# Performance work log

Measured on AMD Instinct MI355X. Metric: run time of the kernel, lower is better.

The kernel has to match this reference:

```python
import math
import jax, jax.numpy as jnp
import numpy as np

B, C, H, W = 8, 256, 32, 32
NH, DK, DV = 8, 32, 32
EPS = 1e-6


def mish(x):
    return x * jnp.tanh(jax.nn.softplus(x))


def grouped_conv1x1(x, w, b, groups):
    # x: (B, Cin, N); w: (Cout, Cin//groups); b: (Cout,)
    Bb, Cin, N = x.shape
    Cout = w.shape[0]
    xg = x.reshape(Bb, groups, Cin // groups, N)
    wg = w.reshape(groups, Cout // groups, Cin // groups)
    y = jnp.einsum('bgin,goi->bgon', xg, wg).reshape(Bb, Cout, N)
    return y + b[None, :, None]


def conv_block(x, w, b, s, beta, groups):
    # 1x1 conv -> BatchNorm (eval: running mean 0 / var 1 => affine) -> Mish
    y = grouped_conv1x1(x, w, b, groups)
    y = s[None, :, None] * y + beta[None, :, None]
    return mish(y)


def setup_inputs() -> dict:
    key = jax.random.key(0)
    ks = jax.random.split(key, 8)
    inp = {
        'x': jax.random.normal(ks[0], (B, C, H, W), dtype=jnp.float32),
        'q_w': jax.random.normal(ks[1], (NH * DK, C // NH), dtype=jnp.float32) * 0.05,
        'q_b': jnp.zeros((NH * DK,), jnp.float32),
        'q_s': jnp.ones((NH * DK,), jnp.float32),
        'q_beta': jnp.zeros((NH * DK,), jnp.float32),
        'k_w': jax.random.normal(ks[2], (NH * DK, C // NH), dtype=jnp.float32) * 0.05,
        'k_b': jnp.zeros((NH * DK,), jnp.float32),
        'k_s': jnp.ones((NH * DK,), jnp.float32),
        'k_beta': jnp.zeros((NH * DK,), jnp.float32),
        'v_w': jax.random.normal(ks[3], (NH * DV, C // NH), dtype=jnp.float32) * 0.05,
        'v_b': jnp.zeros((NH * DV,), jnp.float32),
        'v_s': jnp.ones((NH * DV,), jnp.float32),
        'v_beta': jnp.zeros((NH * DV,), jnp.float32),
        'f_w': jax.random.normal(ks[4], (C, NH * DV), dtype=jnp.float32) * 0.05,
        'f_b': jnp.zeros((C,), jnp.float32),
        'f_s': jnp.ones((C,), jnp.float32),
        'f_beta': jnp.zeros((C,), jnp.float32),
    }
    return inp


def _forward(x, q_w, q_b, q_s, q_beta, k_w, k_b, k_s, k_beta,
             v_w, v_b, v_s, v_beta, f_w, f_b, f_s, f_beta):
    b, c, h, w = x.shape
    n = h * w
    temp = math.sqrt(c / NH)
    xf = x.reshape(b, c, n)

    q = conv_block(xf, q_w, q_b, q_s, q_beta, NH).reshape(b, NH, DK, n) / temp
    k = conv_block(xf, k_w, k_b, k_s, k_beta, NH).reshape(b, NH, DK, n)
    v = conv_block(xf, v_w, v_b, v_s, v_beta, NH).reshape(b, NH, DV, n)

    # cosine-distance attention (all heads vectorized); identical math to the
    # torch broadcast/repeat version but computed via normalized dot products.
    qn = jnp.sqrt(jnp.sum(q * q, axis=2))  # (b, nh, n)
    kn = jnp.sqrt(jnp.sum(k * k, axis=2))
    dot = jnp.einsum('bhdn,bhdm->bhnm', q, k)  # (b, nh, n, n)
    denom = jnp.maximum(qn[:, :, :, None] * kn[:, :, None, :], EPS)
    cos = jnp.clip(dot / denom, -1.0 + 1e-6, 1.0 - 1e-6)
    attn = jax.nn.softmax(1.0 - jnp.arccos(cos) / math.pi, axis=-1)

    # out[..., d, i] = sum_m v[..., d, m] * attn[..., i, m]
    out = jnp.einsum('bhdm,bhnm->bhdn', v, attn).reshape(b, NH * DV, n)

    y = conv_block(out, f_w, f_b, f_s, f_beta, 1).reshape(b, c, h, w) + x

    # extract_attn_map (no_grad in original)
    am = jnp.sum(jnp.mean(attn, axis=1), axis=1)  # (b, n)
    mn = jnp.min(am, axis=1, keepdims=True)
    mx = jnp.max(am, axis=1, keepdims=True)
    am = ((am - mn) / (mx - mn)).reshape(b, h, w)
    return y, jax.lax.stop_gradient(am)


def reference(x, q_w, q_b, q_s, q_beta, k_w, k_b, k_s, k_beta,
              v_w, v_b, v_s, v_beta, f_w, f_b, f_s, f_beta):
    return _forward(x, q_w, q_b, q_s, q_beta, k_w, k_b, k_s, k_beta,
                    v_w, v_b, v_s, v_beta, f_w, f_b, f_s, f_beta)
```

## Files before the change

### kernel.cpp

```cpp
#include <hip/hip_runtime.h>
#include <math.h>

#define B_   8
#define C_   256
#define NH_  8
#define N_   1024
#define LOG2E    1.4426950408889634f

typedef __attribute__((ext_vector_type(8))) short bf16x8;
typedef __attribute__((ext_vector_type(4))) float f32x4;
typedef __attribute__((ext_vector_type(2))) float f32x2;
typedef unsigned short u16;
typedef unsigned int u32;

#define AS1 __attribute__((address_space(1)))
#define AS3 __attribute__((address_space(3)))

__device__ __forceinline__ f32x4 mfma16(bf16x8 a, bf16x8 b, f32x4 c) {
    return __builtin_amdgcn_mfma_f32_16x16x32_bf16(a, b, c, 0, 0, 0);
}
__device__ __forceinline__ u32 bf16r(float x) {
    u32 b = __float_as_uint(x);
    return (b + 0x7fffu + ((b >> 16) & 1u)) >> 16;
}
__device__ __forceinline__ float mish_fast(float x) {
    float e  = __builtin_amdgcn_exp2f(fminf(x, 30.f) * LOG2E);
    float nm = e * (e + 2.f);
    return x * nm * __builtin_amdgcn_rcpf(nm + 2.f);
}
__device__ __forceinline__ f32x2 splat2(float v) { return (f32x2){v, v}; }
__device__ __forceinline__ f32x2 fexp_poly2(f32x2 c) {
    c = __builtin_elementwise_min(
            __builtin_elementwise_max(c, splat2(-0.999999f)), splat2(0.999999f));
    f32x2 u = c * c;
    f32x2 p = __builtin_elementwise_fma(splat2(1.7809920f), u, splat2(-3.7571968f));
    f32x2 q = __builtin_elementwise_fma(splat2(6.3713280f), u, splat2(-15.1427584f));
    p = __builtin_elementwise_fma(p, u, splat2(2.8140000f));
    q = __builtin_elementwise_fma(q, u, splat2(13.1518784f));
    p = __builtin_elementwise_fma(p, u, splat2(-0.8122592f));
    q = __builtin_elementwise_fma(q, u, splat2(-4.8903712f));
    p = __builtin_elementwise_fma(p, u, splat2(0.1705120f));
    q = __builtin_elementwise_fma(q, u, splat2(0.8441120f));
    p = __builtin_elementwise_fma(p, u, splat2(1.6473155f));
    q = __builtin_elementwise_fma(q, u, splat2(0.4936541f));
    return __builtin_elementwise_fma(c, q, p);
}

__global__ __launch_bounds__(256) void qkvpack_kernel(
    const float* __restrict__ x,
    const float* __restrict__ qw, const float* __restrict__ qb2,
    const float* __restrict__ qs, const float* __restrict__ qbeta,
    const float* __restrict__ kw, const float* __restrict__ kb2,
    const float* __restrict__ ks, const float* __restrict__ kbeta,
    const float* __restrict__ vw, const float* __restrict__ vb2,
    const float* __restrict__ vs, const float* __restrict__ vbeta,
    uint4* __restrict__ qpk, uint4* __restrict__ kpk, u16* __restrict__ vbf,
    const float* __restrict__ fw, u16* __restrict__ wbf)
{
    int blk = blockIdx.x;
    if (blk >= 768) {
        int id = (blk - 768) * 1024 + threadIdx.x;
#pragma unroll
        for (int j = 0; j < 4; ++j) { int p = id + j * 256; wbf[p] = (u16)bf16r(fw[p]); }
        return;
    }
    int type = blk >> 8;
    int sub = blk & 255;
    int nt = sub & 3, g = (sub >> 2) & 7, b = sub >> 5;
    int n = nt * 256 + threadIdx.x;
    int bh = b * 8 + g;
    const float* xp = x + ((size_t)b * C_ + g * 32) * N_ + n;
    float xv[32];
#pragma unroll
    for (int i = 0; i < 32; ++i) xv[i] = xp[(size_t)i * N_];

    const float *w, *bb, *sc, *bt;
    if (type == 0)      { w = qw; bb = qb2; sc = qs; bt = qbeta; }
    else if (type == 1) { w = kw; bb = kb2; sc = ks; bt = kbeta; }
    else                { w = vw; bb = vb2; sc = vs; bt = vbeta; }

    float y[32];
#pragma unroll
    for (int co = 0; co < 32; ++co) {
        int cg = g * 32 + co;
        float acc = 0.f;
#pragma unroll
        for (int i = 0; i < 32; ++i)
            acc = fmaf(xv[i], w[cg * 32 + i], acc);
        y[co] = mish_fast(sc[cg] * (acc + bb[cg]) + bt[cg]);
    }

    if (type == 2) {
#pragma unroll
        for (int co = 0; co < 32; ++co)
            vbf[((size_t)bh * 32 + co) * N_ + n] = (u16)bf16r(y[co]);
        return;
    }
    float s2 = 0.f;
#pragma unroll
    for (int d = 0; d < 32; ++d) s2 = fmaf(y[d], y[d], s2);
    float inv = __builtin_amdgcn_rsqf(fmaxf(s2, 1e-24f));
    u32 wp[16];
#pragma unroll
    for (int d = 0; d < 16; ++d)
        wp[d] = bf16r(y[2 * d] * inv) | (bf16r(y[2 * d + 1] * inv) << 16);
    uint4* dst = (type == 0 ? qpk : kpk) + ((size_t)bh * N_ + n) * 4;
#pragma unroll
    for (int j = 0; j < 4; ++j)
        dst[j] = make_uint4(wp[4 * j], wp[4 * j + 1], wp[4 * j + 2], wp[4 * j + 3]);
}

__global__ __launch_bounds__(256) void attn_kernel(
    const u16* __restrict__ qpk, const u16* __restrict__ kpk,
    const u16* __restrict__ vbf,
    u16* __restrict__ aout_bt, float* __restrict__ ampart)
{
    __shared__ __align__(16) u16 Kc[512 * 8];
    __shared__ __align__(16) u16 Vc[512 * 8];
    __shared__ __align__(16) u16 Ps[4][16 * 136];
    __shared__ __align__(16) float amW[N_];

    const int tid  = threadIdx.x;
    const int wave = tid >> 6, lane = tid & 63;
    const int l15 = lane & 15, lg = lane >> 4;
    const int swz = (blockIdx.x & 7) * 128 + (blockIdx.x >> 3);
    const int itile = swz & 15, bh = swz >> 4;
    const int h = bh & 7, bidx = bh >> 3;
    const int i0 = itile * 64;

    const char* ksrc = (const char*)(kpk + (size_t)bh * N_ * 32);
    const char* vsrc = (const char*)(vbf + (size_t)bh * 32 * N_);
    const char* qsrc = (const char*)(qpk + (size_t)bh * N_ * 32);

    for (int j = tid; j < N_; j += 256) amW[j] = 0.f;

    const int kj0 = tid >> 7, km0g = tid & 127;
    const int kj1 = (256 + tid) >> 7, km1g = (256 + tid) & 127;
    const int vd0 = tid >> 4, vg0 = tid & 15;
    const int vd1 = (256 + tid) >> 4, vg1 = (256 + tid) & 15;
    const size_t koff0 = (size_t)km0g * 64 + kj0 * 16;
    const size_t koff1 = (size_t)km1g * 64 + kj1 * 16;
    const size_t voff0 = (size_t)vd0 * 2048 + ((vg0 ^ (vd0 & 7)) << 4);
    const size_t voff1 = (size_t)vd1 * 2048 + ((vg1 ^ (vd1 & 7)) << 4);

    bf16x8 aq = *(const bf16x8*)(qsrc + (size_t)(i0 + wave * 16 + l15) * 64 + lg * 16);

    const char* kfb = (const char*)Kc + lg * 2048 + l15 * 16;

    uint4 kreg0 = *(const uint4*)(ksrc + koff0);
    uint4 kreg1 = *(const uint4*)(ksrc + koff1);
    f32x2 rsL = {0.f, 0.f}, rsH = {0.f, 0.f};
    for (int ch = 0; ch < 8; ++ch) {
        *(uint4*)((char*)Kc + tid * 16)         = kreg0;
        *(uint4*)((char*)Kc + (256 + tid) * 16) = kreg1;
        if (ch < 7) {
            kreg0 = *(const uint4*)(ksrc + (size_t)(ch + 1) * 8192 + koff0);
            kreg1 = *(const uint4*)(ksrc + (size_t)(ch + 1) * 8192 + koff1);
        }
        asm volatile("s_waitcnt lgkmcnt(0)" ::: "memory");
        __builtin_amdgcn_sched_barrier(0);
        __builtin_amdgcn_s_barrier();
        __builtin_amdgcn_sched_barrier(0);
#pragma unroll
        for (int t = 0; t < 8; ++t) {
            bf16x8 bk = *(const bf16x8*)(kfb + t * 256);
            f32x4 cf = {0.f, 0.f, 0.f, 0.f};
            cf = mfma16(aq, bk, cf);
            rsL += fexp_poly2((f32x2){cf[0], cf[1]});
            rsH += fexp_poly2((f32x2){cf[2], cf[3]});
        }
        asm volatile("s_waitcnt lgkmcnt(0)" ::: "memory");
        __builtin_amdgcn_sched_barrier(0);
        __builtin_amdgcn_s_barrier();
        __builtin_amdgcn_sched_barrier(0);
    }
    float rinv[4];
    {
        float rr[4] = {rsL.x, rsL.y, rsH.x, rsH.y};
#pragma unroll
        for (int r = 0; r < 4; ++r) {
            float s = rr[r];
            s += __shfl_xor(s, 1); s += __shfl_xor(s, 2);
            s += __shfl_xor(s, 4); s += __shfl_xor(s, 8);
            rinv[r] = __builtin_amdgcn_rcpf(s);
        }
    }
    f32x2 rinvL = {rinv[0], rinv[1]}, rinvH = {rinv[2], rinv[3]};

    f32x4 o0 = {0.f, 0.f, 0.f, 0.f}, o1 = {0.f, 0.f, 0.f, 0.f};
    char*       psw = (char*)&Ps[wave][0] + lg * 1088 + l15 * 2;
    const char* pab = (const char*)&Ps[wave][0] + l15 * 272 + lg * 16;
    const char* vfb = (const char*)Vc + l15 * 256;
    const int   vkey = l15 & 7;

    kreg0 = *(const uint4*)(ksrc + koff0);
    kreg1 = *(const uint4*)(ksrc + koff1);
    uint4 vreg0 = *(const uint4*)(vsrc + voff0);
    uint4 vreg1 = *(const uint4*)(vsrc + voff1);

    for (int ch = 0; ch < 8; ++ch) {
        int m0 = ch * 128;
        *(uint4*)((char*)Kc + tid * 16)         = kreg0;
        *(uint4*)((char*)Kc + (256 + tid) * 16) = kreg1;
        *(uint4*)((char*)Vc + tid * 16)         = vreg0;
        *(uint4*)((char*)Vc + (256 + tid) * 16) = vreg1;
        if (ch < 7) {
            kreg0 = *(const uint4*)(ksrc + (size_t)(ch + 1) * 8192 + koff0);
            kreg1 = *(const uint4*)(ksrc + (size_t)(ch + 1) * 8192 + koff1);
            vreg0 = *(const uint4*)(vsrc + (size_t)(ch + 1) * 256 + voff0);
            vreg1 = *(const uint4*)(vsrc + (size_t)(ch + 1) * 256 + voff1);
        }
        asm volatile("s_waitcnt lgkmcnt(0)" ::: "memory");
        __builtin_amdgcn_sched_barrier(0);
        __builtin_amdgcn_s_barrier();
        __builtin_amdgcn_sched_barrier(0);

#pragma unroll
        for (int t = 0; t < 8; ++t) {
            bf16x8 bk = *(const bf16x8*)(kfb + t * 256);
            f32x4 cf = {0.f, 0.f, 0.f, 0.f};
            cf = mfma16(aq, bk, cf);
            f32x2 fL = fexp_poly2((f32x2){cf[0], cf[1]});
            f32x2 fH = fexp_poly2((f32x2){cf[2], cf[3]});
            *(u16*)(psw + 0 * 272 + t * 32) = (u16)bf16r(fL.x);
            *(u16*)(psw + 1 * 272 + t * 32) = (u16)bf16r(fL.y);
            *(u16*)(psw + 2 * 272 + t * 32) = (u16)bf16r(fH.x);
            *(u16*)(psw + 3 * 272 + t * 32) = (u16)bf16r(fH.y);
            f32x2 cs2 = fL * rinvL;
            cs2 = __builtin_elementwise_fma(fH, rinvH, cs2);
            float csum = cs2.x + cs2.y;
            csum += __shfl_xor(csum, 16);
            csum += __shfl_xor(csum, 32);
            if (lane < 16) atomicAdd(&amW[m0 + t * 16 + l15], csum);
        }
        asm volatile("s_waitcnt lgkmcnt(0)" ::: "memory");
        __builtin_amdgcn_sched_barrier(0);
#pragma unroll
        for (int kss = 0; kss < 4; ++kss) {
            bf16x8 pa = *(const bf16x8*)(pab + kss * 64);
            const char* va = vfb + (((kss * 4 + lg) ^ vkey) << 4);
            bf16x8 v0 = *(const bf16x8*)va;
            bf16x8 v1 = *(const bf16x8*)(va + 4096);
            o0 = mfma16(pa, v0, o0);
            o1 = mfma16(pa, v1, o1);
        }
        asm volatile("s_waitcnt lgkmcnt(0)" ::: "memory");
        __builtin_amdgcn_sched_barrier(0);
        __builtin_amdgcn_s_barrier();
        __builtin_amdgcn_sched_barrier(0);
    }
    __syncthreads();

    {
        u16* oT = (u16*)Ps;
#pragma unroll
        for (int r = 0; r < 4; ++r) {
            int irow = wave * 16 + lg * 4 + r;
            oT[irow * 40 + l15]      = (u16)bf16r(o0[r] * rinv[r]);
            oT[irow * 40 + 16 + l15] = (u16)bf16r(o1[r] * rinv[r]);
        }
    }
    __syncthreads();
    {
        const u16* oT = (const u16*)Ps;
        int row = tid >> 2, c4 = tid & 3;
        uint4 val = *(const uint4*)((const char*)oT + row * 80 + c4 * 16);
        int n = i0 + row;
        int g = h * 4 + c4;
        size_t dst = ((size_t)(bidx * N_ + n) << 9) + ((size_t)((g ^ (row & 7)) << 4));
        *(uint4*)((char*)aout_bt + dst) = val;
    }
#pragma unroll
    for (int j2 = 0; j2 < 4; ++j2)
        ampart[(size_t)swz * N_ + tid + 256 * j2] = amW[tid + 256 * j2];
}

__global__ __launch_bounds__(256) void fconv_kernel(
    const u16* __restrict__ aout_bt, const u16* __restrict__ wbf,
    const float* __restrict__ x,
    const float* __restrict__ fs, const float* __restrict__ fb,
    const float* __restrict__ fbeta, float* __restrict__ y,
    const float* __restrict__ ampart, float* __restrict__ outAm)
{
    __shared__ __align__(16) u16 As[32 * 256];
    __shared__ float rmn[256], rmx[256];
    const int tid = threadIdx.x;

    if (blockIdx.x >= 256) {
        int b = blockIdx.x - 256;
        const float* base = ampart + (size_t)b * 128 * N_;
        float s[4] = {0.f, 0.f, 0.f, 0.f};
        for (int p = 0; p < 128; ++p) {
#pragma unroll
            for (int c2 = 0; c2 < 4; ++c2)
                s[c2] += base[(size_t)p * N_ + tid + 256 * c2];
        }
        float mn = fminf(fminf(s[0], s[1]), fminf(s[2], s[3]));
        float mx = fmaxf(fmaxf(s[0], s[1]), fmaxf(s[2], s[3]));
        rmn[tid] = mn; rmx[tid] = mx;
        __syncthreads();
        for (int off = 128; off >= 1; off >>= 1) {
            if (tid < off) {
                rmn[tid] = fminf(rmn[tid], rmn[tid + off]);
                rmx[tid] = fmaxf(rmx[tid], rmx[tid + off]);
            }
            __syncthreads();
        }
        mn = rmn[0]; mx = rmx[0];
        float inv = 1.f / (mx - mn);
#pragma unroll
        for (int c2 = 0; c2 < 4; ++c2)
            outAm[(size_t)b * N_ + tid + 256 * c2] = (s[c2] - mn) * inv;
        return;
    }

    const int wave = tid >> 6, lane = tid & 63;
    const int l15 = lane & 15, lg = lane >> 4;
    const int b  = blockIdx.x >> 5;
    const int n0 = (blockIdx.x & 31) * 32;

    const char* asrc = (const char*)aout_bt + ((size_t)(b * N_ + n0) << 9);
#pragma unroll
    for (int p = 0; p < 4; ++p) {
        int g = p * 256 + wave * 64 + lane;
        __builtin_amdgcn_global_load_lds(
            (const AS1 void*)(asrc + g * 16),
            (AS3 void*)((char*)As + ((p * 256 + wave * 64) << 4)), 16, 0, 0);
    }
    __syncthreads();

    f32x4 acc[4][2];
#pragma unroll
    for (int f = 0; f < 4; ++f)
#pragma unroll
        for (int fn = 0; fn < 2; ++fn) acc[f][fn] = (f32x4){0.f, 0.f, 0.f, 0.f};

    const int cobase = wave * 64;
#pragma unroll
    for (int kk = 0; kk < 8; ++kk) {
        bf16x8 af[2];
#pragma unroll
        for (int fn = 0; fn < 2; ++fn) {
            int nf = fn * 16 + l15;
            af[fn] = *(const bf16x8*)((const char*)As + nf * 512 +
                                      (((kk * 4 + lg) ^ (nf & 7)) << 4));
        }
#pragma unroll
        for (int f = 0; f < 4; ++f) {
            bf16x8 wf = *(const bf16x8*)(wbf + (size_t)(cobase + f * 16 + l15) * 256 + kk * 32 + lg * 8);
            acc[f][0] = mfma16(wf, af[0], acc[f][0]);
            acc[f][1] = mfma16(wf, af[1], acc[f][1]);
        }
    }

#pragma unroll
    for (int f = 0; f < 4; ++f) {
#pragma unroll
        for (int r = 0; r < 4; ++r) {
            int co = cobase + f * 16 + lg * 4 + r;
            float sc = fs[co], bb = fb[co], bt = fbeta[co];
#pragma unroll
            for (int fn = 0; fn < 2; ++fn) {
                int n = n0 + fn * 16 + l15;
                size_t oid = ((size_t)(b * C_ + co) << 10) + n;
                y[oid] = mish_fast(sc * (acc[f][fn][r] + bb) + bt) + x[oid];
            }
        }
    }
}

extern "C" void kernel_launch(void* const* d_in, const int* in_sizes, int n_in,
                              void* d_out, int out_size, void* d_ws, size_t ws_size,
                              hipStream_t stream)
{
    const float* x     = (const float*)d_in[0];
    const float* q_w   = (const float*)d_in[1];
    const float* q_b   = (const float*)d_in[2];
    const float* q_s   = (const float*)d_in[3];
    const float* q_be  = (const float*)d_in[4];
    const float* k_w   = (const float*)d_in[5];
    const float* k_b   = (const float*)d_in[6];
    const float* k_s   = (const float*)d_in[7];
    const float* k_be  = (const float*)d_in[8];
    const float* v_w   = (const float*)d_in[9];
    const float* v_b   = (const float*)d_in[10];
    const float* v_s   = (const float*)d_in[11];
    const float* v_be  = (const float*)d_in[12];
    const float* f_w   = (const float*)d_in[13];
    const float* f_b   = (const float*)d_in[14];
    const float* f_s   = (const float*)d_in[15];
    const float* f_be  = (const float*)d_in[16];

    float* y_out  = (float*)d_out;
    float* am_out = (float*)d_out + (size_t)B_ * C_ * N_;

    char* w = (char*)d_ws;
    u16*   qpk     = (u16*)w;    w += (size_t)B_ * NH_ * N_ * 64;
    u16*   kpk     = (u16*)w;    w += (size_t)B_ * NH_ * N_ * 64;
    u16*   vbf     = (u16*)w;    w += (size_t)B_ * C_ * N_ * 2;
    u16*   aout_bt = (u16*)w;    w += (size_t)B_ * N_ * C_ * 2;
    float* ampart  = (float*)w;  w += (size_t)B_ * NH_ * 16 * N_ * 4;
    u16*   wbf     = (u16*)w;

    qkvpack_kernel<<<832, 256, 0, stream>>>(
        x, q_w, q_b, q_s, q_be, k_w, k_b, k_s, k_be,
        v_w, v_b, v_s, v_be, (uint4*)qpk, (uint4*)kpk, vbf, f_w, wbf);

    attn_kernel<<<B_ * NH_ * 16, 256, 0, stream>>>(
        qpk, kpk, vbf, aout_bt, ampart);

    fconv_kernel<<<264, 256, 0, stream>>>(
        aout_bt, wbf, x, f_s, f_b, f_be, y_out, ampart, am_out);
}
```

Measured before the change: 104.5 us.

## Double-buffer K/V tiles in LDS with direct global_load_lds transfers

Replaces the register-staged global-to-LDS copies of K and V chunks with `__builtin_amdgcn_global_load_lds` DMA into double-buffered LDS tiles. The next chunk is prefetched into the alternate buffer while the current one is consumed. This cuts the two barriers per chunk down to one vmcnt wait plus barrier. The aim is to save VGPRs and VALU store instructions and to overlap memory latency with the MFMA and exp work. In exchange it doubles the K/V LDS footprint, which may lower occupancy, and the new scheme depends on careful vmcnt/barrier ordering being correct.

```diff
diff --git a/kernel.cpp b/kernel.cpp
--- a/kernel.cpp
+++ b/kernel.cpp
@@ -115,8 +115,8 @@
     const u16* __restrict__ vbf,
     u16* __restrict__ aout_bt, float* __restrict__ ampart)
 {
-    __shared__ __align__(16) u16 Kc[512 * 8];
-    __shared__ __align__(16) u16 Vc[512 * 8];
+    __shared__ __align__(16) u16 Kb[2][512 * 8];
+    __shared__ __align__(16) u16 Vb[2][512 * 8];
     __shared__ __align__(16) u16 Ps[4][16 * 136];
     __shared__ __align__(16) float amW[N_];
 
@@ -134,33 +134,44 @@
 
     for (int j = tid; j < N_; j += 256) amW[j] = 0.f;
 
-    const int kj0 = tid >> 7, km0g = tid & 127;
-    const int kj1 = (256 + tid) >> 7, km1g = (256 + tid) & 127;
-    const int vd0 = tid >> 4, vg0 = tid & 15;
-    const int vd1 = (256 + tid) >> 4, vg1 = (256 + tid) & 15;
-    const size_t koff0 = (size_t)km0g * 64 + kj0 * 16;
-    const size_t koff1 = (size_t)km1g * 64 + kj1 * 16;
+    const int g0 = wave * 64 + lane, g1 = 256 + wave * 64 + lane;
+    const size_t koff0 = (size_t)(g0 & 127) * 64 + (size_t)(g0 >> 7) * 16;
+    const size_t koff1 = (size_t)(g1 & 127) * 64 + (size_t)(g1 >> 7) * 16;
+    const int vd0 = g0 >> 4, vg0 = g0 & 15, vd1 = g1 >> 4, vg1 = g1 & 15;
     const size_t voff0 = (size_t)vd0 * 2048 + ((vg0 ^ (vd0 & 7)) << 4);
     const size_t voff1 = (size_t)vd1 * 2048 + ((vg1 ^ (vd1 & 7)) << 4);
+    const int dst0 = (wave * 64) << 4, dst1 = (256 + wave * 64) << 4;
+
+#define STAGE_K(ch, bsel) do {                                               \
+    __builtin_amdgcn_global_load_lds(                                        \
+        (const AS1 void*)(ksrc + (size_t)(ch) * 8192 + koff0),               \
+        (AS3 void*)((char*)Kb[bsel] + dst0), 16, 0, 0);                      \
+    __builtin_amdgcn_global_load_lds(                                        \
+        (const AS1 void*)(ksrc + (size_t)(ch) * 8192 + koff1),               \
+        (AS3 void*)((char*)Kb[bsel] + dst1), 16, 0, 0);                      \
+} while (0)
+#define STAGE_V(ch, bsel) do {                                               \
+    __builtin_amdgcn_global_load_lds(                                        \
+        (const AS1 void*)(vsrc + (size_t)(ch) * 256 + voff0),                \
+        (AS3 void*)((char*)Vb[bsel] + dst0), 16, 0, 0);                      \
+    __builtin_amdgcn_global_load_lds(                                        \
+        (const AS1 void*)(vsrc + (size_t)(ch) * 256 + voff1),                \
+        (AS3 void*)((char*)Vb[bsel] + dst1), 16, 0, 0);                      \
+} while (0)
 
     bf16x8 aq = *(const bf16x8*)(qsrc + (size_t)(i0 + wave * 16 + l15) * 64 + lg * 16);
 
-    const char* kfb = (const char*)Kc + lg * 2048 + l15 * 16;
-
-    uint4 kreg0 = *(const uint4*)(ksrc + koff0);
-    uint4 kreg1 = *(const uint4*)(ksrc + koff1);
+    const int kfo = lg * 2048 + l15 * 16;
+
+    STAGE_K(0, 0);
+    asm volatile("s_waitcnt vmcnt(0)" ::: "memory");
+    __builtin_amdgcn_s_barrier();
+    __builtin_amdgcn_sched_barrier(0);
     f32x2 rsL = {0.f, 0.f}, rsH = {0.f, 0.f};
     for (int ch = 0; ch < 8; ++ch) {
-        *(uint4*)((char*)Kc + tid * 16)         = kreg0;
-        *(uint4*)((char*)Kc + (256 + tid) * 16) = kreg1;
-        if (ch < 7) {
-            kreg0 = *(const uint4*)(ksrc + (size_t)(ch + 1) * 8192 + koff0);
-            kreg1 = *(const uint4*)(ksrc + (size_t)(ch + 1) * 8192 + koff1);
-        }
-        asm volatile("s_waitcnt lgkmcnt(0)" ::: "memory");
-        __builtin_amdgcn_sched_barrier(0);
-        __builtin_amdgcn_s_barrier();
-        __builtin_amdgcn_sched_barrier(0);
+        int cur = ch & 1;
+        if (ch < 7) STAGE_K(ch + 1, cur ^ 1);
+        const char* kfb = (const char*)Kb[cur] + kfo;
 #pragma unroll
         for (int t = 0; t < 8; ++t) {
             bf16x8 bk = *(const bf16x8*)(kfb + t * 256);
@@ -169,10 +180,11 @@
             rsL += fexp_poly2((f32x2){cf[0], cf[1]});
             rsH += fexp_poly2((f32x2){cf[2], cf[3]});
         }
-        asm volatile("s_waitcnt lgkmcnt(0)" ::: "memory");
-        __builtin_amdgcn_sched_barrier(0);
-        __builtin_amdgcn_s_barrier();
-        __builtin_amdgcn_sched_barrier(0);
+        if (ch < 7) {
+            asm volatile("s_waitcnt vmcnt(0)" ::: "memory");
+            __builtin_amdgcn_s_barrier();
+            __builtin_amdgcn_sched_barrier(0);
+        }
     }
     float rinv[4];
     {
@@ -190,30 +202,21 @@
     f32x4 o0 = {0.f, 0.f, 0.f, 0.f}, o1 = {0.f, 0.f, 0.f, 0.f};
     char*       psw = (char*)&Ps[wave][0] + lg * 1088 + l15 * 2;
     const char* pab = (const char*)&Ps[wave][0] + l15 * 272 + lg * 16;
-    const char* vfb = (const char*)Vc + l15 * 256;
+    const int   vfo = l15 * 256;
     const int   vkey = l15 & 7;
 
-    kreg0 = *(const uint4*)(ksrc + koff0);
-    kreg1 = *(const uint4*)(ksrc + koff1);
-    uint4 vreg0 = *(const uint4*)(vsrc + voff0);
-    uint4 vreg1 = *(const uint4*)(vsrc + voff1);
+    STAGE_K(0, 0);
+    STAGE_V(0, 0);
+    asm volatile("s_waitcnt vmcnt(0)" ::: "memory");
+    __builtin_amdgcn_s_barrier();
+    __builtin_amdgcn_sched_barrier(0);
 
     for (int ch = 0; ch < 8; ++ch) {
+        int cur = ch & 1;
         int m0 = ch * 128;
-        *(uint4*)((char*)Kc + tid * 16)         = kreg0;
-        *(uint4*)((char*)Kc + (256 + tid) * 16) = kreg1;
-        *(uint4*)((char*)Vc + tid * 16)         = vreg0;
-        *(uint4*)((char*)Vc + (256 + tid) * 16) = vreg1;
-        if (ch < 7) {
-            kreg0 = *(const uint4*)(ksrc + (size_t)(ch + 1) * 8192 + koff0);
-            kreg1 = *(const uint4*)(ksrc + (size_t)(ch + 1) * 8192 + koff1);
-            vreg0 = *(const uint4*)(vsrc + (size_t)(ch + 1) * 256 + voff0);
-            vreg1 = *(const uint4*)(vsrc + (size_t)(ch + 1) * 256 + voff1);
-        }
-        asm volatile("s_waitcnt lgkmcnt(0)" ::: "memory");
-        __builtin_amdgcn_sched_barrier(0);
-        __builtin_amdgcn_s_barrier();
-        __builtin_amdgcn_sched_barrier(0);
+        if (ch < 7) { STAGE_K(ch + 1, cur ^ 1); STAGE_V(ch + 1, cur ^ 1); }
+        const char* kfb = (const char*)Kb[cur] + kfo;
+        const char* vfb = (const char*)Vb[cur] + vfo;
 
 #pragma unroll
         for (int t = 0; t < 8; ++t) {
@@ -244,10 +247,11 @@
             o0 = mfma16(pa, v0, o0);
             o1 = mfma16(pa, v1, o1);
         }
-        asm volatile("s_waitcnt lgkmcnt(0)" ::: "memory");
-        __builtin_amdgcn_sched_barrier(0);
-        __builtin_amdgcn_s_barrier();
-        __builtin_amdgcn_sched_barrier(0);
+        if (ch < 7) {
+            asm volatile("s_waitcnt vmcnt(0)" ::: "memory");
+            __builtin_amdgcn_s_barrier();
+            __builtin_amdgcn_sched_barrier(0);
+        }
     }
     __syncthreads();
 
@@ -273,6 +277,8 @@
 #pragma unroll
     for (int j2 = 0; j2 < 4; ++j2)
         ampart[(size_t)swz * N_ + tid + 256 * j2] = amW[tid + 256 * j2];
+#undef STAGE_K
+#undef STAGE_V
 }
 
 __global__ __launch_bounds__(256) void fconv_kernel(
```

Measured after the change: 118.9 us. 1.14x slower.

## Split softmax row-sum pass into separate kernel with halved key range

Applied to the files above, without the earlier changes.

Moves the first pass of the attention kernel, which computes the softmax denominators, into its own rowsum kernel. That kernel splits the key range in half across twice as many blocks and loads K with double-buffered global_load_lds. The attention kernel then reads the two partial sums and goes straight to the PV pass. This aims to raise parallelism for the sum pass and shorten the attention kernel, at the cost of an extra launch, a small workspace buffer, and reading Q/K again.

```diff
diff --git a/kernel.cpp b/kernel.cpp
--- a/kernel.cpp
+++ b/kernel.cpp
@@ -110,9 +110,81 @@
         dst[j] = make_uint4(wp[4 * j], wp[4 * j + 1], wp[4 * j + 2], wp[4 * j + 3]);
 }
 
+__global__ __launch_bounds__(256) void rowsum_kernel(
+    const u16* __restrict__ qpk, const u16* __restrict__ kpk,
+    float* __restrict__ rowsumP)
+{
+    __shared__ __align__(16) u16 Kb[2][512 * 8];
+
+    const int tid  = threadIdx.x;
+    const int wave = tid >> 6, lane = tid & 63;
+    const int l15 = lane & 15, lg = lane >> 4;
+    const int swz = (blockIdx.x & 7) * 256 + (blockIdx.x >> 3);
+    const int mh = swz & 1, itile = (swz >> 1) & 15, bh = swz >> 5;
+    const int i0 = itile * 64;
+    const int m00 = mh * 512;
+
+    const char* ksrc = (const char*)(kpk + (size_t)bh * N_ * 32);
+    const char* qsrc = (const char*)(qpk + (size_t)bh * N_ * 32);
+
+    const size_t koff0 = (size_t)(tid & 127) * 64 + (size_t)(tid >> 7) * 16;
+    const size_t koff1 = (size_t)((256 + tid) & 127) * 64 + (size_t)((256 + tid) >> 7) * 16;
+
+    bf16x8 aq = *(const bf16x8*)(qsrc + (size_t)(i0 + wave * 16 + l15) * 64 + lg * 16);
+    const int kfo = lg * 2048 + l15 * 16;
+
+#define RS_STAGE(ch, bsel) do {                                              \
+    __builtin_amdgcn_global_load_lds(                                        \
+        (const AS1 void*)(ksrc + (size_t)(m00 + (ch) * 128) * 64 + koff0),   \
+        (AS3 void*)((char*)Kb[bsel] + (tid << 4)), 16, 0, 0);                \
+    __builtin_amdgcn_global_load_lds(                                        \
+        (const AS1 void*)(ksrc + (size_t)(m00 + (ch) * 128) * 64 + koff1),   \
+        (AS3 void*)((char*)Kb[bsel] + ((256 + tid) << 4)), 16, 0, 0);        \
+} while (0)
+
+    RS_STAGE(0, 0);
+    asm volatile("s_waitcnt vmcnt(0)" ::: "memory");
+    __builtin_amdgcn_s_barrier();
+    __builtin_amdgcn_sched_barrier(0);
+
+    f32x2 rsL = {0.f, 0.f}, rsH = {0.f, 0.f};
+    for (int ch = 0; ch < 4; ++ch) {
+        if (ch < 3) RS_STAGE(ch + 1, (ch + 1) & 1);
+        const char* kfb = (const char*)Kb[ch & 1] + kfo;
+#pragma unroll
+        for (int t = 0; t < 8; ++t) {
+            bf16x8 bk = *(const bf16x8*)(kfb + t * 256);
+            f32x4 cf = {0.f, 0.f, 0.f, 0.f};
+            cf = mfma16(aq, bk, cf);
+            rsL += fexp_poly2((f32x2){cf[0], cf[1]});
+            rsH += fexp_poly2((f32x2){cf[2], cf[3]});
+        }
+        if (ch < 3) {
+            asm volatile("s_waitcnt vmcnt(0)" ::: "memory");
+            __builtin_amdgcn_s_barrier();
+            __builtin_amdgcn_sched_barrier(0);
+        }
+    }
+#undef RS_STAGE
+    float rr[4] = {rsL.x, rsL.y, rsH.x, rsH.y};
+#pragma unroll
+    for (int r = 0; r < 4; ++r) {
+        float s = rr[r];
+        s += __shfl_xor(s, 1); s += __shfl_xor(s, 2);
+        s += __shfl_xor(s, 4); s += __shfl_xor(s, 8);
+        rr[r] = s;
+    }
+    if (l15 == 0) {
+#pragma unroll
+        for (int r = 0; r < 4; ++r)
+            rowsumP[(size_t)mh * (B_ * NH_ * N_) + (size_t)bh * N_ +
+                    i0 + wave * 16 + lg * 4 + r] = rr[r];
+    }
+}
+
 __global__ __launch_bounds__(256) void attn_kernel(
     const u16* __restrict__ qpk, const u16* __restrict__ kpk,
-    const u16* __restrict__ vbf,
+    const u16* __restrict__ vbf, const float* __restrict__ rowsumP,
     u16* __restrict__ aout_bt, float* __restrict__ ampart)
 {
     __shared__ __align__(16) u16 Kc[512 * 8];
@@ -147,43 +219,12 @@
 
     const char* kfb = (const char*)Kc + lg * 2048 + l15 * 16;
 
-    uint4 kreg0 = *(const uint4*)(ksrc + koff0);
-    uint4 kreg1 = *(const uint4*)(ksrc + koff1);
-    f32x2 rsL = {0.f, 0.f}, rsH = {0.f, 0.f};
-    for (int ch = 0; ch < 8; ++ch) {
-        *(uint4*)((char*)Kc + tid * 16)         = kreg0;
-        *(uint4*)((char*)Kc + (256 + tid) * 16) = kreg1;
-        if (ch < 7) {
-            kreg0 = *(const uint4*)(ksrc + (size_t)(ch + 1) * 8192 + koff0);
-            kreg1 = *(const uint4*)(ksrc + (size_t)(ch + 1) * 8192 + koff1);
-        }
-        asm volatile("s_waitcnt lgkmcnt(0)" ::: "memory");
-        __builtin_amdgcn_sched_barrier(0);
-        __builtin_amdgcn_s_barrier();
-        __builtin_amdgcn_sched_barrier(0);
-#pragma unroll
-        for (int t = 0; t < 8; ++t) {
-            bf16x8 bk = *(const bf16x8*)(kfb + t * 256);
-            f32x4 cf = {0.f, 0.f, 0.f, 0.f};
-            cf = mfma16(aq, bk, cf);
-            rsL += fexp_poly2((f32x2){cf[0], cf[1]});
-            rsH += fexp_poly2((f32x2){cf[2], cf[3]});
-        }
-        asm volatile("s_waitcnt lgkmcnt(0)" ::: "memory");
-        __builtin_amdgcn_sched_barrier(0);
-        __builtin_amdgcn_s_barrier();
-        __builtin_amdgcn_sched_barrier(0);
-    }
     float rinv[4];
     {
-        float rr[4] = {rsL.x, rsL.y, rsH.x, rsH.y};
-#pragma unroll
-        for (int r = 0; r < 4; ++r) {
-            float s = rr[r];
-            s += __shfl_xor(s, 1); s += __shfl_xor(s, 2);
-            s += __shfl_xor(s, 4); s += __shfl_xor(s, 8);
-            rinv[r] = __builtin_amdgcn_rcpf(s);
-        }
+        const float* rp = rowsumP + (size_t)bh * N_ + i0 + wave * 16 + lg * 4;
+#pragma unroll
+        for (int r = 0; r < 4; ++r)
+            rinv[r] = __builtin_amdgcn_rcpf(rp[r] + rp[B_ * NH_ * N_ + r]);
     }
     f32x2 rinvL = {rinv[0], rinv[1]}, rinvH = {rinv[2], rinv[3]};
 
@@ -193,8 +234,8 @@
     const char* vfb = (const char*)Vc + l15 * 256;
     const int   vkey = l15 & 7;
 
-    kreg0 = *(const uint4*)(ksrc + koff0);
-    kreg1 = *(const uint4*)(ksrc + koff1);
+    uint4 kreg0 = *(const uint4*)(ksrc + koff0);
+    uint4 kreg1 = *(const uint4*)(ksrc + koff1);
     uint4 vreg0 = *(const uint4*)(vsrc + voff0);
     uint4 vreg1 = *(const uint4*)(vsrc + voff1);
 
@@ -400,14 +441,17 @@
     u16*   vbf     = (u16*)w;    w += (size_t)B_ * C_ * N_ * 2;
     u16*   aout_bt = (u16*)w;    w += (size_t)B_ * N_ * C_ * 2;
     float* ampart  = (float*)w;  w += (size_t)B_ * NH_ * 16 * N_ * 4;
-    u16*   wbf     = (u16*)w;
+    u16*   wbf     = (u16*)w;    w += (size_t)C_ * C_ * 2;
+    float* rowsumP = (float*)w;
 
     qkvpack_kernel<<<832, 256, 0, stream>>>(
         x, q_w, q_b, q_s, q_be, k_w, k_b, k_s, k_be,
         v_w, v_b, v_s, v_be, (uint4*)qpk, (uint4*)kpk, vbf, f_w, wbf);
 
+    rowsum_kernel<<<B_ * NH_ * 16 * 2, 256, 0, stream>>>(qpk, kpk, rowsumP);
+
     attn_kernel<<<B_ * NH_ * 16, 256, 0, stream>>>(
-        qpk, kpk, vbf, aout_bt, ampart);
+        qpk, kpk, vbf, rowsumP, aout_bt, ampart);
 
     fconv_kernel<<<264, 256, 0, stream>>>(
         aout_bt, wbf, x, f_s, f_b, f_be, y_out, ampart, am_out);
```

Result: slower. 116.4 us (+11.3%).
